# Performance work log

Hardware: AMD Instinct MI355X
Metric: run time of the kernel (lower is better)

## Reference

```python
import jax, jax.numpy as jnp
import numpy as np

N = 100000   # num_nodes
E = 1600000  # num_edges
D = 64       # input_dim
H = 64       # hidden_dim
G = 64       # num graphs in batch


def gcn_conv(x, row, col, ew, W, b):
    """PyG GCNConv with edge_weight and self-loops (weight 1.0).
    out = D^{-1/2} (A + I) D^{-1/2} X W + b, aggregating src->dst (row->col)."""
    h = x @ W  # [N, H]
    deg = jax.ops.segment_sum(ew, col, num_segments=N) + 1.0  # self-loop weight 1
    dinv = jnp.where(deg > 0, jax.lax.rsqrt(deg), 0.0)
    norm = dinv[row] * ew * dinv[col]                     # [E]
    agg = jax.ops.segment_sum(h[row] * norm[:, None], col, num_segments=N)
    out = agg + h * (dinv * dinv)[:, None]                # self-loop term
    return out + b


def setup_inputs() -> dict:
    key = jax.random.key(0)
    ks = jax.random.split(key, 20)
    def w(i, shape, fan_in):
        return (jax.random.uniform(ks[i], shape, jnp.float32) * 2.0 - 1.0) / np.sqrt(fan_in)
    inp = {
        "x": jax.random.normal(ks[0], (N, D), jnp.float32),
        "edge_index": jax.random.randint(ks[1], (2, E), 0, N, dtype=jnp.int64),
        "edge_attr": jax.random.uniform(ks[2], (E, 1), jnp.float32),
        "batch": jnp.sort(jax.random.randint(ks[3], (N,), 0, G, dtype=jnp.int64)),
        # GCN layers
        "W0": w(4, (D, H), D), "b0": w(5, (H,), D),
        "W1": w(6, (H, H), H), "b1": w(7, (H,), H),
        "W2": w(8, (H, H), H), "b2": w(9, (H,), H),
        "fc1_w": w(10, (H, H // 2), H), "fc1_b": w(11, (H // 2,), H),
        "fc2_w": w(12, (H // 2, 1), H // 2), "fc2_b": w(13, (1,), H // 2),
        "out_w": w(14, (1, 1), 1), "out_b": w(15, (1,), 1),
    }
    return inp


def reference(x, edge_index, edge_attr, batch, W0, b0, W1, b1, W2, b2,
              fc1_w, fc1_b, fc2_w, fc2_b, out_w, out_b):
    row, col = edge_index[0], edge_index[1]
    ew = edge_attr.reshape(-1)  # edge_attr.view(-1) used as edge_weight
    h = gcn_conv(x, row, col, ew, W0, b0)
    h = jax.nn.relu(h)  # dropout is identity in eval mode
    h = gcn_conv(h, row, col, ew, W1, b1)
    h = jax.nn.relu(h)
    h = gcn_conv(h, row, col, ew, W2, b2)  # no relu after last conv
    # global_mean_pool over batch indices
    sums = jax.ops.segment_sum(h, batch, num_segments=G)            # [G, H]
    cnts = jax.ops.segment_sum(jnp.ones((N,), h.dtype), batch, num_segments=G)
    g = sums / jnp.maximum(cnts, 1.0)[:, None]
    g = jax.nn.relu(g @ fc1_w + fc1_b)
    g = g @ fc2_w + fc2_b                  # [G, 1]
    return g @ out_w + out_b               # [G, 1]
```

## Files before the change

### kernel.cpp

```cpp
#include <hip/hip_runtime.h>
#include <hip/hip_bf16.h>

#define NN 100000
#define NE 1600000
#define DIM 64
#define NG 64

#define NBUK 391
#define EPB 4096
#define NBLK 391

static __device__ __forceinline__ unsigned short bf16bits(float v) {
    __hip_bfloat16 b = __float2bfloat16(v);
    return *reinterpret_cast<unsigned short*>(&b);
}
static __device__ __forceinline__ float bfbits2f(unsigned short u) {
    unsigned int x = ((unsigned int)u) << 16;
    return __uint_as_float(x);
}
static __device__ __forceinline__ void bf2x(unsigned int u, float& lo, float& hi) {
    lo = __uint_as_float(u << 16);
    hi = __uint_as_float(u & 0xFFFF0000u);
}
static __device__ __forceinline__ unsigned csr_pack(int r, float nm) {
    unsigned u = __float_as_uint(nm);
    unsigned nb = ((u + 0x8000u) >> 16) & 0x7FFFu;
    return ((unsigned)r << 15) | nb;
}
static __device__ __forceinline__ float csr_nrm(unsigned u) {
    return __uint_as_float((u & 0x7FFFu) << 16);
}

__global__ __launch_bounds__(1024) void k_ghist2(const int* __restrict__ col,
                                                 int* __restrict__ hist2d,
                                                 int* gcnt, int E) {
    __shared__ int hist[NBUK];
    int t = threadIdx.x;
    for (int i = t; i < NBUK; i += 1024) hist[i] = 0;
    __syncthreads();
    int e0 = blockIdx.x * EPB, e1 = min(e0 + EPB, E);
    for (int e = e0 + t; e < e1; e += 1024) atomicAdd(&hist[col[e] >> 8], 1);
    __syncthreads();
    for (int i = t; i < NBUK; i += 1024) {
        int c = hist[i];
        hist2d[blockIdx.x * NBUK + i] = c;
        if (c) atomicAdd(&gcnt[i], c);
    }
}

__global__ __launch_bounds__(256) void k_gscan(const int* __restrict__ gcnt,
                                               int* __restrict__ boff,
                                               float* __restrict__ sums,
                                               float* __restrict__ cntf) {
    __shared__ int sm[256];
    int t = threadIdx.x;
    for (int i = t; i < NG * DIM; i += 256) sums[i] = 0.f;
    if (t < NG) cntf[t] = 0.f;
    int v0 = (2 * t < NBUK) ? gcnt[2 * t] : 0;
    int v1 = (2 * t + 1 < NBUK) ? gcnt[2 * t + 1] : 0;
    int s = v0 + v1;
    sm[t] = s;
    __syncthreads();
    for (int off = 1; off < 256; off <<= 1) {
        int tmp = (t >= off) ? sm[t - off] : 0;
        __syncthreads();
        sm[t] += tmp;
        __syncthreads();
    }
    int run = sm[t] - s;
    if (2 * t < NBUK) boff[2 * t] = run;
    run += v0;
    if (2 * t + 1 < NBUK) boff[2 * t + 1] = run;
    if (t == 255) boff[NBUK] = run + v1;
}

__global__ __launch_bounds__(256) void k_colscan(const int* __restrict__ hist2d,
                                                 const int* __restrict__ boff,
                                                 int* __restrict__ base2d,
                                                 const float* __restrict__ x,
                                                 unsigned short* __restrict__ xb) {
    __shared__ int sm[256];
    int b = blockIdx.x, t = threadIdx.x;
    int v0 = (2 * t < NBLK) ? hist2d[(size_t)(2 * t) * NBUK + b] : 0;
    int v1 = (2 * t + 1 < NBLK) ? hist2d[(size_t)(2 * t + 1) * NBUK + b] : 0;
    int s = v0 + v1;
    sm[t] = s;
    __syncthreads();
    for (int off = 1; off < 256; off <<= 1) {
        int tmp = (t >= off) ? sm[t - off] : 0;
        __syncthreads();
        sm[t] += tmp;
        __syncthreads();
    }
    int run = boff[b] + sm[t] - s;
    if (2 * t < NBLK) base2d[(size_t)(2 * t) * NBUK + b] = run;
    run += v0;
    if (2 * t + 1 < NBLK) base2d[(size_t)(2 * t + 1) * NBUK + b] = run;
    const int NQ = NN * DIM / 4;
    const int per = (NQ + NBLK - 1) / NBLK;
    int q0 = b * per, q1 = min(q0 + per, NQ);
    for (int i = q0 + t; i < q1; i += 256) {
        float4 v = ((const float4*)x)[i];
        ushort4 o;
        o.x = bf16bits(v.x);
        o.y = bf16bits(v.y);
        o.z = bf16bits(v.z);
        o.w = bf16bits(v.w);
        ((ushort4*)xb)[i] = o;
    }
}

__global__ __launch_bounds__(1024) void k_part1v2(const int* __restrict__ row,
                                                  const int* __restrict__ col,
                                                  const float* __restrict__ ew,
                                                  const int* __restrict__ base2d,
                                                  int2* __restrict__ binned, int E) {
    __shared__ int cur[NBUK];
    int t = threadIdx.x;
    for (int i = t; i < NBUK; i += 1024) cur[i] = base2d[(size_t)blockIdx.x * NBUK + i];
    __syncthreads();
    int e0 = blockIdx.x * EPB, e1 = min(e0 + EPB, E);
    for (int e = e0 + t; e < e1; e += 1024) {
        int c = col[e];
        int b = c >> 8, cl = c & 255;
        int p = atomicAdd(&cur[b], 1);
        binned[p] = make_int2((cl << 17) | row[e], __float_as_int(ew[e]));
    }
}

__global__ __launch_bounds__(256) void k_p2a(const int2* __restrict__ binned,
                                             const int* __restrict__ boff,
                                             float* __restrict__ dinv,
                                             int* __restrict__ rowptr) {
    int b = blockIdx.x, t = threadIdx.x;
    __shared__ unsigned int dsum[256];
    __shared__ int ncnt[256];
    __shared__ int sm[256];
    dsum[t] = 0;
    ncnt[t] = 0;
    __syncthreads();
    int e0 = boff[b], e1 = boff[b + 1];
    for (int e = e0 + t; e < e1; e += 256) {
        int2 v = binned[e];
        int cl = v.x >> 17;
        atomicAdd(&ncnt[cl], 1);
        unsigned int fx = (unsigned int)__float2uint_rn(__int_as_float(v.y) * 16777216.0f);
        atomicAdd(&dsum[cl], fx);
    }
    __syncthreads();
    int c = ncnt[t];
    sm[t] = c;
    __syncthreads();
    for (int off = 1; off < 256; off <<= 1) {
        int tmp = (t >= off) ? sm[t - off] : 0;
        __syncthreads();
        sm[t] += tmp;
        __syncthreads();
    }
    int node = b * 256 + t;
    if (node < NN) {
        rowptr[node] = e0 + sm[t] - c;
        dinv[node] = rsqrtf(1.0f + (float)dsum[t] * (1.0f / 16777216.0f));
    }
    if (b == 0 && t == 0) rowptr[NN] = NE;
}

__global__ __launch_bounds__(256) void k_p2b(const int2* __restrict__ binned,
                                             const int* __restrict__ boff,
                                             const float* __restrict__ dinv,
                                             const int* __restrict__ rowptr,
                                             unsigned* __restrict__ csr) {
    int b = blockIdx.x, t = threadIdx.x;
    __shared__ int ncur[256];
    __shared__ float ldin[256];
    int node = b * 256 + t;
    ncur[t] = (node < NN) ? rowptr[node] : 0;
    ldin[t] = (node < NN) ? dinv[node] : 0.f;
    __syncthreads();
    int e0 = boff[b], e1 = boff[b + 1];
    for (int e = e0 + t; e < e1; e += 256) {
        int2 v = binned[e];
        int cl = v.x >> 17, r = v.x & 0x1FFFF;
        float nm = dinv[r] * __int_as_float(v.y) * ldin[cl];
        int p = atomicAdd(&ncur[cl], 1);
        csr[p] = csr_pack(r, nm);
    }
}

__global__ __launch_bounds__(256) void k_gather5(const int* __restrict__ rowptr,
                                                 const unsigned* __restrict__ csr,
                                                 const uint4* __restrict__ h8,
                                                 const float* __restrict__ dinv,
                                                 uint4* __restrict__ out, int n) {
    int tid = threadIdx.x;
    int node = blockIdx.x * 16 + (tid >> 4);
    if (node >= n) return;
    int l = tid & 15;
    int g2 = l >> 3, sub = l & 7;
    float acc[8];
#pragma unroll
    for (int i = 0; i < 8; ++i) acc[i] = 0.f;
    if (g2 == 0) {
        float di = dinv[node];
        float s = di * di;
        uint4 v = h8[(size_t)node * 8 + sub];
        float lo, hi;
        bf2x(v.x, lo, hi); acc[0] = lo * s; acc[1] = hi * s;
        bf2x(v.y, lo, hi); acc[2] = lo * s; acc[3] = hi * s;
        bf2x(v.z, lo, hi); acc[4] = lo * s; acc[5] = hi * s;
        bf2x(v.w, lo, hi); acc[6] = lo * s; acc[7] = hi * s;
    }
    int e1 = rowptr[node + 1];
    int e = rowptr[node] + g2;
    unsigned p[4];
#pragma unroll
    for (int i = 0; i < 4; ++i) {
        p[i] = 0u;
        if (e + 2 * i < e1) p[i] = csr[e + 2 * i];
    }
    while (e < e1) {
        uint4 r[4];
#pragma unroll
        for (int i = 0; i < 4; ++i) {
            r[i] = make_uint4(0u, 0u, 0u, 0u);
            if (e + 2 * i < e1) r[i] = h8[(size_t)(p[i] >> 15) * 8 + sub];
        }
        int en = e + 8;
        unsigned q[4];
#pragma unroll
        for (int i = 0; i < 4; ++i) {
            q[i] = 0u;
            if (en + 2 * i < e1) q[i] = csr[en + 2 * i];
        }
#pragma unroll
        for (int i = 0; i < 4; ++i) {
            float nm = csr_nrm(p[i]);
            float lo, hi;
            bf2x(r[i].x, lo, hi); acc[0] = fmaf(lo, nm, acc[0]); acc[1] = fmaf(hi, nm, acc[1]);
            bf2x(r[i].y, lo, hi); acc[2] = fmaf(lo, nm, acc[2]); acc[3] = fmaf(hi, nm, acc[3]);
            bf2x(r[i].z, lo, hi); acc[4] = fmaf(lo, nm, acc[4]); acc[5] = fmaf(hi, nm, acc[5]);
            bf2x(r[i].w, lo, hi); acc[6] = fmaf(lo, nm, acc[6]); acc[7] = fmaf(hi, nm, acc[7]);
        }
#pragma unroll
        for (int i = 0; i < 4; ++i) p[i] = q[i];
        e = en;
    }
#pragma unroll
    for (int i = 0; i < 8; ++i) acc[i] += __shfl_xor(acc[i], 8);
    if (g2 == 0) {
        uint4 o;
        o.x = ((unsigned int)bf16bits(acc[1]) << 16) | bf16bits(acc[0]);
        o.y = ((unsigned int)bf16bits(acc[3]) << 16) | bf16bits(acc[2]);
        o.z = ((unsigned int)bf16bits(acc[5]) << 16) | bf16bits(acc[4]);
        o.w = ((unsigned int)bf16bits(acc[7]) << 16) | bf16bits(acc[6]);
        out[(size_t)node * 8 + sub] = o;
    }
}

__global__ __launch_bounds__(256, 4) void k_gemm64v3(const ushort4* __restrict__ in,
                                                     const float* __restrict__ W,
                                                     const float* __restrict__ b,
                                                     ushort4* __restrict__ out, int n) {
    __shared__ float sW[64][64];
    __shared__ float sX[64][68];
    int tid = threadIdx.x;
#pragma unroll
    for (int i = 0; i < 4; ++i) {
        int q = tid + i * 256;
        ((float4*)&sW[0][0])[q] = ((const float4*)W)[q];
    }
    int base = blockIdx.x * 64;
#pragma unroll
    for (int i = 0; i < 4; ++i) {
        int idx = tid + i * 256;
        int r = idx >> 4, q = idx & 15;
        int node = base + r;
        float4 f = make_float4(0.f, 0.f, 0.f, 0.f);
        if (node < n) {
            ushort4 v = in[(size_t)node * 16 + q];
            f.x = bfbits2f(v.x);
            f.y = bfbits2f(v.y);
            f.z = bfbits2f(v.z);
            f.w = bfbits2f(v.w);
        }
        *(float4*)&sX[r][q * 4] = f;
    }
    __syncthreads();
    int ng = tid >> 4;
    int dg = tid & 15;
    float acc[4][4];
#pragma unroll
    for (int i = 0; i < 4; ++i)
#pragma unroll
        for (int j = 0; j < 4; ++j) acc[i][j] = 0.f;
#pragma unroll 4
    for (int k4 = 0; k4 < 16; ++k4) {
        float4 xr[4];
#pragma unroll
        for (int i = 0; i < 4; ++i) xr[i] = *(const float4*)&sX[ng * 4 + i][k4 * 4];
        float4 wc[4];
#pragma unroll
        for (int j = 0; j < 4; ++j) wc[j] = *(const float4*)&sW[k4 * 4 + j][dg * 4];
#pragma unroll
        for (int i = 0; i < 4; ++i) {
            acc[i][0] = fmaf(xr[i].x, wc[0].x, acc[i][0]);
            acc[i][1] = fmaf(xr[i].x, wc[0].y, acc[i][1]);
            acc[i][2] = fmaf(xr[i].x, wc[0].z, acc[i][2]);
            acc[i][3] = fmaf(xr[i].x, wc[0].w, acc[i][3]);
            acc[i][0] = fmaf(xr[i].y, wc[1].x, acc[i][0]);
            acc[i][1] = fmaf(xr[i].y, wc[1].y, acc[i][1]);
            acc[i][2] = fmaf(xr[i].y, wc[1].z, acc[i][2]);
            acc[i][3] = fmaf(xr[i].y, wc[1].w, acc[i][3]);
            acc[i][0] = fmaf(xr[i].z, wc[2].x, acc[i][0]);
            acc[i][1] = fmaf(xr[i].z, wc[2].y, acc[i][1]);
            acc[i][2] = fmaf(xr[i].z, wc[2].z, acc[i][2]);
            acc[i][3] = fmaf(xr[i].z, wc[2].w, acc[i][3]);
            acc[i][0] = fmaf(xr[i].w, wc[3].x, acc[i][0]);
            acc[i][1] = fmaf(xr[i].w, wc[3].y, acc[i][1]);
            acc[i][2] = fmaf(xr[i].w, wc[3].z, acc[i][2]);
            acc[i][3] = fmaf(xr[i].w, wc[3].w, acc[i][3]);
        }
    }
    float4 bv = ((const float4*)b)[dg];
#pragma unroll
    for (int i = 0; i < 4; ++i) {
        int node = base + ng * 4 + i;
        if (node < n) {
            ushort4 o;
            o.x = bf16bits(fmaxf(acc[i][0] + bv.x, 0.f));
            o.y = bf16bits(fmaxf(acc[i][1] + bv.y, 0.f));
            o.z = bf16bits(fmaxf(acc[i][2] + bv.z, 0.f));
            o.w = bf16bits(fmaxf(acc[i][3] + bv.w, 0.f));
            out[(size_t)node * 16 + dg] = o;
        }
    }
}

#define PB3 512
__global__ __launch_bounds__(256) void k_pool3(const int* __restrict__ batch,
                                               const uint4* __restrict__ h8,
                                               float* sums, float* cnt, int n) {
    __shared__ float gsum[64][65];
    __shared__ float gcl[64];
    int t = threadIdx.x;
    for (int i = t; i < 64 * 65; i += 256) (&gsum[0][0])[i] = 0.f;
    if (t < 64) gcl[t] = 0.f;
    __syncthreads();
    int base = blockIdx.x * PB3;
    int end = min(base + PB3, n);
    int g0 = batch[base];
    int cl = t >> 3, sub = t & 7;
    float acc[8];
#pragma unroll
    for (int i = 0; i < 8; ++i) acc[i] = 0.f;
    int gcur = -1, runlen = 0;
    for (int node = base + cl; node < end; node += 32) {
        int g = batch[node];
        if (g != gcur) {
            if (gcur >= 0) {
                int gl = gcur - g0;
#pragma unroll
                for (int i = 0; i < 8; ++i) atomicAdd(&gsum[gl][sub * 8 + i], acc[i]);
                if (sub == 0) atomicAdd(&gcl[gl], (float)runlen);
#pragma unroll
                for (int i = 0; i < 8; ++i) acc[i] = 0.f;
            }
            gcur = g;
            runlen = 0;
        }
        uint4 v = h8[(size_t)node * 8 + sub];
        float lo, hi;
        bf2x(v.x, lo, hi); acc[0] += lo; acc[1] += hi;
        bf2x(v.y, lo, hi); acc[2] += lo; acc[3] += hi;
        bf2x(v.z, lo, hi); acc[4] += lo; acc[5] += hi;
        bf2x(v.w, lo, hi); acc[6] += lo; acc[7] += hi;
        runlen++;
    }
    if (gcur >= 0) {
        int gl = gcur - g0;
#pragma unroll
        for (int i = 0; i < 8; ++i) atomicAdd(&gsum[gl][sub * 8 + i], acc[i]);
        if (sub == 0) atomicAdd(&gcl[gl], (float)runlen);
    }
    __syncthreads();
    int g1 = batch[end - 1];
    int ngr = g1 - g0 + 1;
    for (int idx = t; idx < ngr * 64; idx += 256) {
        int gl = idx >> 6, d = idx & 63;
        float v = gsum[gl][d];
        if (v != 0.f) atomicAdd(&sums[(g0 + gl) * DIM + d], v);
    }
    if (t < ngr) {
        float c = gcl[t];
        if (c != 0.f) atomicAdd(&cnt[g0 + t], c);
    }
}

__global__ __launch_bounds__(64) void k_head(const float* __restrict__ sums,
                                             const float* __restrict__ cnt,
                                             const float* __restrict__ W2,
                                             const float* __restrict__ b2,
                                             const float* __restrict__ fc1w,
                                             const float* __restrict__ fc1b,
                                             const float* __restrict__ fc2w,
                                             const float* __restrict__ fc2b,
                                             const float* __restrict__ ow,
                                             const float* __restrict__ ob,
                                             float* __restrict__ out) {
    int g = blockIdx.x;
    int t = threadIdx.x;
    __shared__ float gv[64];
    __shared__ float tv[64];
    float c = fmaxf(cnt[g], 1.0f);
    gv[t] = sums[g * DIM + t] / c;
    __syncthreads();
    float acc2 = b2[t];
#pragma unroll
    for (int k = 0; k < 64; ++k) acc2 = fmaf(gv[k], W2[k * 64 + t], acc2);
    tv[t] = acc2;
    __syncthreads();
    float r = 0.0f;
    if (t < 32) {
        float acc = fc1b[t];
#pragma unroll
        for (int k = 0; k < 64; ++k) acc = fmaf(tv[k], fc1w[k * 32 + t], acc);
        acc = fmaxf(acc, 0.0f);
        r = acc * fc2w[t];
    }
#pragma unroll
    for (int off = 16; off; off >>= 1) r += __shfl_down(r, off);
    if (t == 0) out[g] = (r + fc2b[0]) * ow[0] + ob[0];
}

extern "C" void kernel_launch(void* const* d_in, const int* in_sizes, int n_in,
                              void* d_out, int out_size, void* d_ws, size_t ws_size,
                              hipStream_t stream) {
    const float* x   = (const float*)d_in[0];
    const int* eidx  = (const int*)d_in[1];
    const float* ew  = (const float*)d_in[2];
    const int* batch = (const int*)d_in[3];
    const float* W0  = (const float*)d_in[4];
    const float* b0  = (const float*)d_in[5];
    const float* W1  = (const float*)d_in[6];
    const float* b1  = (const float*)d_in[7];
    const float* W2  = (const float*)d_in[8];
    const float* b2  = (const float*)d_in[9];
    const float* fc1w = (const float*)d_in[10];
    const float* fc1b = (const float*)d_in[11];
    const float* fc2w = (const float*)d_in[12];
    const float* fc2b = (const float*)d_in[13];
    const float* ow   = (const float*)d_in[14];
    const float* ob   = (const float*)d_in[15];
    float* out = (float*)d_out;

    const int* row = eidx;
    const int* col = eidx + NE;

    char* ws = (char*)d_ws;
    int2* binned           = (int2*)ws;               ws += sizeof(int2) * NE;
    unsigned* csr          = (unsigned*)ws;           ws += sizeof(unsigned) * NE;
    __hip_bfloat16* Xb     = (__hip_bfloat16*)ws;     ws += sizeof(__hip_bfloat16) * (size_t)NN * DIM;
    __hip_bfloat16* Hb     = (__hip_bfloat16*)ws;     ws += sizeof(__hip_bfloat16) * (size_t)NN * DIM;
    int*   hist2d          = (int*)ws;                ws += sizeof(int) * (size_t)NBLK * NBUK;
    int*   base2d          = (int*)ws;                ws += sizeof(int) * (size_t)NBLK * NBUK;
    float* dinv            = (float*)ws;              ws += sizeof(float) * NN;
    int*   rowptr          = (int*)ws;                ws += sizeof(int) * (NN + 1);
    int*   gcnt            = (int*)ws;                ws += sizeof(int) * (NBUK + 1);
    int*   boff            = (int*)ws;                ws += sizeof(int) * (NBUK + 1);
    float* sums            = (float*)ws;              ws += sizeof(float) * NG * DIM;
    float* cntf            = (float*)ws;              ws += sizeof(float) * NG;

    hipMemsetAsync(gcnt, 0, sizeof(int) * NBUK, stream);
    k_ghist2<<<NBLK, 1024, 0, stream>>>(col, hist2d, gcnt, NE);
    k_gscan<<<1, 256, 0, stream>>>(gcnt, boff, sums, cntf);
    k_colscan<<<NBUK, 256, 0, stream>>>(hist2d, boff, base2d, x, (unsigned short*)Xb);
    k_part1v2<<<NBLK, 1024, 0, stream>>>(row, col, ew, base2d, binned, NE);
    k_p2a<<<NBUK, 256, 0, stream>>>(binned, boff, dinv, rowptr);
    k_p2b<<<NBUK, 256, 0, stream>>>(binned, boff, dinv, rowptr, csr);

    int gemm_blocks = (NN + 63) / 64;
    int gath_blocks = (NN + 15) / 16;

    k_gather5<<<gath_blocks, 256, 0, stream>>>(rowptr, csr, (const uint4*)Xb, dinv, (uint4*)Hb, NN);
    k_gemm64v3<<<gemm_blocks, 256, 0, stream>>>((const ushort4*)Hb, W0, b0, (ushort4*)Xb, NN);
    k_gather5<<<gath_blocks, 256, 0, stream>>>(rowptr, csr, (const uint4*)Xb, dinv, (uint4*)Hb, NN);
    k_gemm64v3<<<gemm_blocks, 256, 0, stream>>>((const ushort4*)Hb, W1, b1, (ushort4*)Xb, NN);
    k_gather5<<<gath_blocks, 256, 0, stream>>>(rowptr, csr, (const uint4*)Xb, dinv, (uint4*)Hb, NN);

    k_pool3<<<(NN + PB3 - 1) / PB3, 256, 0, stream>>>(batch, (const uint4*)Hb, sums, cntf, NN);
    k_head<<<NG, 64, 0, stream>>>(sums, cntf, W2, b2, fc1w, fc1b, fc2w, fc2b, ow, ob, out);
}
```

Measured before the change: 224.6 us.

## Fuse neighbor gather with following dense GEMM into single kernel per layer

Result: faster. 197.9 us (-11.9%).

```diff
diff --git a/kernel.cpp b/kernel.cpp
--- a/kernel.cpp
+++ b/kernel.cpp
@@ -187,6 +187,107 @@
     }
 }
 
+__global__ __launch_bounds__(256, 7) void k_gg(const int* __restrict__ rowptr,
+                                               const unsigned* __restrict__ csr,
+                                               const uint4* __restrict__ h8,
+                                               const float* __restrict__ dinv,
+                                               const float* __restrict__ W,
+                                               const float* __restrict__ b,
+                                               ushort4* __restrict__ out) {
+    __shared__ float sW[64][64];
+    __shared__ float sX[16][68];
+    int tid = threadIdx.x;
+#pragma unroll
+    for (int i = 0; i < 4; ++i) {
+        int q = tid + i * 256;
+        ((float4*)&sW[0][0])[q] = ((const float4*)W)[q];
+    }
+    int node = blockIdx.x * 16 + (tid >> 4);
+    int l = tid & 15;
+    int g2 = l >> 3, sub = l & 7;
+    float acc[8];
+#pragma unroll
+    for (int i = 0; i < 8; ++i) acc[i] = 0.f;
+    if (g2 == 0) {
+        float di = dinv[node];
+        float s = di * di;
+        uint4 v = h8[(size_t)node * 8 + sub];
+        float lo, hi;
+        bf2x(v.x, lo, hi); acc[0] = lo * s; acc[1] = hi * s;
+        bf2x(v.y, lo, hi); acc[2] = lo * s; acc[3] = hi * s;
+        bf2x(v.z, lo, hi); acc[4] = lo * s; acc[5] = hi * s;
+        bf2x(v.w, lo, hi); acc[6] = lo * s; acc[7] = hi * s;
+    }
+    int e1 = rowptr[node + 1];
+    int e = rowptr[node] + g2;
+    unsigned p[4];
+#pragma unroll
+    for (int i = 0; i < 4; ++i) {
+        p[i] = 0u;
+        if (e + 2 * i < e1) p[i] = csr[e + 2 * i];
+    }
+    while (e < e1) {
+        uint4 r[4];
+#pragma unroll
+        for (int i = 0; i < 4; ++i) {
+            r[i] = make_uint4(0u, 0u, 0u, 0u);
+            if (e + 2 * i < e1) r[i] = h8[(size_t)(p[i] >> 15) * 8 + sub];
+        }
+        int en = e + 8;
+        unsigned q[4];
+#pragma unroll
+        for (int i = 0; i < 4; ++i) {
+            q[i] = 0u;
+            if (en + 2 * i < e1) q[i] = csr[en + 2 * i];
+        }
+#pragma unroll
+        for (int i = 0; i < 4; ++i) {
+            float nm = csr_nrm(p[i]);
+            float lo, hi;
+            bf2x(r[i].x, lo, hi); acc[0] = fmaf(lo, nm, acc[0]); acc[1] = fmaf(hi, nm, acc[1]);
+            bf2x(r[i].y, lo, hi); acc[2] = fmaf(lo, nm, acc[2]); acc[3] = fmaf(hi, nm, acc[3]);
+            bf2x(r[i].z, lo, hi); acc[4] = fmaf(lo, nm, acc[4]); acc[5] = fmaf(hi, nm, acc[5]);
+            bf2x(r[i].w, lo, hi); acc[6] = fmaf(lo, nm, acc[6]); acc[7] = fmaf(hi, nm, acc[7]);
+        }
+#pragma unroll
+        for (int i = 0; i < 4; ++i) p[i] = q[i];
+        e = en;
+    }
+#pragma unroll
+    for (int i = 0; i < 8; ++i) acc[i] += __shfl_xor(acc[i], 8);
+    if (g2 == 0) {
+        int c = tid >> 4;
+        *(float4*)&sX[c][sub * 8 + 0] = make_float4(acc[0], acc[1], acc[2], acc[3]);
+        *(float4*)&sX[c][sub * 8 + 4] = make_float4(acc[4], acc[5], acc[6], acc[7]);
+    }
+    __syncthreads();
+    int nl = tid >> 4, dg = tid & 15;
+    float a0 = 0.f, a1 = 0.f, a2 = 0.f, a3 = 0.f;
+#pragma unroll 4
+    for (int k4 = 0; k4 < 16; ++k4) {
+        float4 xr = *(const float4*)&sX[nl][k4 * 4];
+        float4 w0 = *(const float4*)&sW[k4 * 4 + 0][dg * 4];
+        float4 w1 = *(const float4*)&sW[k4 * 4 + 1][dg * 4];
+        float4 w2 = *(const float4*)&sW[k4 * 4 + 2][dg * 4];
+        float4 w3 = *(const float4*)&sW[k4 * 4 + 3][dg * 4];
+        a0 = fmaf(xr.x, w0.x, a0); a1 = fmaf(xr.x, w0.y, a1);
+        a2 = fmaf(xr.x, w0.z, a2); a3 = fmaf(xr.x, w0.w, a3);
+        a0 = fmaf(xr.y, w1.x, a0); a1 = fmaf(xr.y, w1.y, a1);
+        a2 = fmaf(xr.y, w1.z, a2); a3 = fmaf(xr.y, w1.w, a3);
+        a0 = fmaf(xr.z, w2.x, a0); a1 = fmaf(xr.z, w2.y, a1);
+        a2 = fmaf(xr.z, w2.z, a2); a3 = fmaf(xr.z, w2.w, a3);
+        a0 = fmaf(xr.w, w3.x, a0); a1 = fmaf(xr.w, w3.y, a1);
+        a2 = fmaf(xr.w, w3.z, a2); a3 = fmaf(xr.w, w3.w, a3);
+    }
+    float4 bv = ((const float4*)b)[dg];
+    ushort4 o;
+    o.x = bf16bits(fmaxf(a0 + bv.x, 0.f));
+    o.y = bf16bits(fmaxf(a1 + bv.y, 0.f));
+    o.z = bf16bits(fmaxf(a2 + bv.z, 0.f));
+    o.w = bf16bits(fmaxf(a3 + bv.w, 0.f));
+    out[(size_t)(blockIdx.x * 16 + nl) * 16 + dg] = o;
+}
+
 __global__ __launch_bounds__(256) void k_gather5(const int* __restrict__ rowptr,
                                                  const unsigned* __restrict__ csr,
                                                  const uint4* __restrict__ h8,
@@ -254,85 +355,6 @@
         o.z = ((unsigned int)bf16bits(acc[5]) << 16) | bf16bits(acc[4]);
         o.w = ((unsigned int)bf16bits(acc[7]) << 16) | bf16bits(acc[6]);
         out[(size_t)node * 8 + sub] = o;
-    }
-}
-
-__global__ __launch_bounds__(256, 4) void k_gemm64v3(const ushort4* __restrict__ in,
-                                                     const float* __restrict__ W,
-                                                     const float* __restrict__ b,
-                                                     ushort4* __restrict__ out, int n) {
-    __shared__ float sW[64][64];
-    __shared__ float sX[64][68];
-    int tid = threadIdx.x;
-#pragma unroll
-    for (int i = 0; i < 4; ++i) {
-        int q = tid + i * 256;
-        ((float4*)&sW[0][0])[q] = ((const float4*)W)[q];
-    }
-    int base = blockIdx.x * 64;
-#pragma unroll
-    for (int i = 0; i < 4; ++i) {
-        int idx = tid + i * 256;
-        int r = idx >> 4, q = idx & 15;
-        int node = base + r;
-        float4 f = make_float4(0.f, 0.f, 0.f, 0.f);
-        if (node < n) {
-            ushort4 v = in[(size_t)node * 16 + q];
-            f.x = bfbits2f(v.x);
-            f.y = bfbits2f(v.y);
-            f.z = bfbits2f(v.z);
-            f.w = bfbits2f(v.w);
-        }
-        *(float4*)&sX[r][q * 4] = f;
-    }
-    __syncthreads();
-    int ng = tid >> 4;
-    int dg = tid & 15;
-    float acc[4][4];
-#pragma unroll
-    for (int i = 0; i < 4; ++i)
-#pragma unroll
-        for (int j = 0; j < 4; ++j) acc[i][j] = 0.f;
-#pragma unroll 4
-    for (int k4 = 0; k4 < 16; ++k4) {
-        float4 xr[4];
-#pragma unroll
-        for (int i = 0; i < 4; ++i) xr[i] = *(const float4*)&sX[ng * 4 + i][k4 * 4];
-        float4 wc[4];
-#pragma unroll
-        for (int j = 0; j < 4; ++j) wc[j] = *(const float4*)&sW[k4 * 4 + j][dg * 4];
-#pragma unroll
-        for (int i = 0; i < 4; ++i) {
-            acc[i][0] = fmaf(xr[i].x, wc[0].x, acc[i][0]);
-            acc[i][1] = fmaf(xr[i].x, wc[0].y, acc[i][1]);
-            acc[i][2] = fmaf(xr[i].x, wc[0].z, acc[i][2]);
-            acc[i][3] = fmaf(xr[i].x, wc[0].w, acc[i][3]);
-            acc[i][0] = fmaf(xr[i].y, wc[1].x, acc[i][0]);
-            acc[i][1] = fmaf(xr[i].y, wc[1].y, acc[i][1]);
-            acc[i][2] = fmaf(xr[i].y, wc[1].z, acc[i][2]);
-            acc[i][3] = fmaf(xr[i].y, wc[1].w, acc[i][3]);
-            acc[i][0] = fmaf(xr[i].z, wc[2].x, acc[i][0]);
-            acc[i][1] = fmaf(xr[i].z, wc[2].y, acc[i][1]);
-            acc[i][2] = fmaf(xr[i].z, wc[2].z, acc[i][2]);
-            acc[i][3] = fmaf(xr[i].z, wc[2].w, acc[i][3]);
-            acc[i][0] = fmaf(xr[i].w, wc[3].x, acc[i][0]);
-            acc[i][1] = fmaf(xr[i].w, wc[3].y, acc[i][1]);
-            acc[i][2] = fmaf(xr[i].w, wc[3].z, acc[i][2]);
-            acc[i][3] = fmaf(xr[i].w, wc[3].w, acc[i][3]);
-        }
-    }
-    float4 bv = ((const float4*)b)[dg];
-#pragma unroll
-    for (int i = 0; i < 4; ++i) {
-        int node = base + ng * 4 + i;
-        if (node < n) {
-            ushort4 o;
-            o.x = bf16bits(fmaxf(acc[i][0] + bv.x, 0.f));
-            o.y = bf16bits(fmaxf(acc[i][1] + bv.y, 0.f));
-            o.z = bf16bits(fmaxf(acc[i][2] + bv.z, 0.f));
-            o.w = bf16bits(fmaxf(acc[i][3] + bv.w, 0.f));
-            out[(size_t)node * 16 + dg] = o;
-        }
     }
 }
 
@@ -478,15 +500,12 @@
     k_p2a<<<NBUK, 256, 0, stream>>>(binned, boff, dinv, rowptr);
     k_p2b<<<NBUK, 256, 0, stream>>>(binned, boff, dinv, rowptr, csr);
 
-    int gemm_blocks = (NN + 63) / 64;
-    int gath_blocks = (NN + 15) / 16;
-
-    k_gather5<<<gath_blocks, 256, 0, stream>>>(rowptr, csr, (const uint4*)Xb, dinv, (uint4*)Hb, NN);
-    k_gemm64v3<<<gemm_blocks, 256, 0, stream>>>((const ushort4*)Hb, W0, b0, (ushort4*)Xb, NN);
-    k_gather5<<<gath_blocks, 256, 0, stream>>>(rowptr, csr, (const uint4*)Xb, dinv, (uint4*)Hb, NN);
-    k_gemm64v3<<<gemm_blocks, 256, 0, stream>>>((const ushort4*)Hb, W1, b1, (ushort4*)Xb, NN);
-    k_gather5<<<gath_blocks, 256, 0, stream>>>(rowptr, csr, (const uint4*)Xb, dinv, (uint4*)Hb, NN);
-
+    int gg_blocks = NN / 16;
+
+    k_gg<<<gg_blocks, 256, 0, stream>>>(rowptr, csr, (const uint4*)Xb, dinv, W0, b0, (ushort4*)Hb);
+    k_gg<<<gg_blocks, 256, 0, stream>>>(rowptr, csr, (const uint4*)Hb, dinv, W1, b1, (ushort4*)Xb);
+
+    k_gather5<<<gg_blocks, 256, 0, stream>>>(rowptr, csr, (const uint4*)Xb, dinv, (uint4*)Hb, NN);
     k_pool3<<<(NN + PB3 - 1) / PB3, 256, 0, stream>>>(batch, (const uint4*)Hb, sums, cntf, NN);
     k_head<<<NG, 64, 0, stream>>>(sums, cntf, W2, b2, fc1w, fc1b, fc2w, fc2b, ow, ob, out);
 }
```
